# Performance work log

Measured on AMD Instinct MI355X. Metric: run time of the kernel, lower is better.

## Reference

```python
import jax, jax.numpy as jnp
import numpy as np

CHUNK = 64

def _l2norm(x, eps=1e-6):
    return x / jnp.sqrt(jnp.sum(x * x, axis=-1, keepdims=True) + eps)

def setup_inputs() -> dict:
    key = jax.random.key(0)
    ks = jax.random.split(key, 5)
    B, S, H, Dk, Dv = 2, 4096, 16, 128, 128
    q = jax.random.normal(ks[0], (B, S, H, Dk), jnp.float32)
    k = jax.random.normal(ks[1], (B, S, H, Dk), jnp.float32)
    v = jax.random.normal(ks[2], (B, S, H, Dv), jnp.float32)
    g = -jax.random.uniform(ks[3], (B, S, H), jnp.float32)          # log-decay, negative
    beta = jax.random.uniform(ks[4], (B, S, H), jnp.float32)        # (0,1) learning rate
    return {"query": q, "key": k, "value": v, "g": g, "beta": beta}

def reference(query, key, value, g, beta):
    C = CHUNK
    init_dtype = query.dtype
    # [b, s, h, d] -> [b, h, s, d], fp32
    q = jnp.transpose(query, (0, 2, 1, 3)).astype(jnp.float32)
    k = jnp.transpose(key, (0, 2, 1, 3)).astype(jnp.float32)
    v = jnp.transpose(value, (0, 2, 1, 3)).astype(jnp.float32)
    gg = jnp.transpose(g, (0, 2, 1)).astype(jnp.float32)
    bb = jnp.transpose(beta, (0, 2, 1)).astype(jnp.float32)
    # use_qk_l2norm_in_kernel=True
    q = _l2norm(q)
    k = _l2norm(k)
    gg = jnp.clip(gg, -20.0, 20.0)
    B, H, S, Dk = k.shape
    Dv = v.shape[-1]
    pad = (-S) % C
    if pad:
        q = jnp.pad(q, ((0, 0), (0, 0), (0, pad), (0, 0)))
        k = jnp.pad(k, ((0, 0), (0, 0), (0, pad), (0, 0)))
        v = jnp.pad(v, ((0, 0), (0, 0), (0, pad), (0, 0)))
        gg = jnp.pad(gg, ((0, 0), (0, 0), (0, pad)))
        bb = jnp.pad(bb, ((0, 0), (0, 0), (0, pad)))
    T = S + pad
    N = T // C
    q = q * (1.0 / np.sqrt(Dk).astype(np.float32))
    v_beta = v * bb[..., None]
    k_beta = k * bb[..., None]
    # chunk: [b, h, n, c, d]
    qc = q.reshape(B, H, N, C, Dk)
    kc = k.reshape(B, H, N, C, Dk)
    vc = v.reshape(B, H, N, C, Dv)
    kbc = k_beta.reshape(B, H, N, C, Dk)
    vbc = v_beta.reshape(B, H, N, C, Dv)
    gc = jnp.cumsum(gg.reshape(B, H, N, C), axis=-1)
    tril = jnp.tril(jnp.ones((C, C), bool))
    strict = jnp.tril(jnp.ones((C, C), bool), -1)
    # decay_mask[i,j] = exp(g_i - g_j) on lower triangle (incl diag), else 0
    gd = gc[..., :, None] - gc[..., None, :]
    decay = jnp.where(tril, jnp.exp(jnp.where(tril, gd, 0.0)), 0.0)
    # UT transform: torch's in-place row loop computes Tm = (I - A)^{-1} with
    # A = -(k_beta @ k^T * decay) on the strictly lower triangle.
    kk = jnp.einsum('bhnik,bhnjk->bhnij', kbc, kc)
    A = jnp.where(strict, -(kk * decay), 0.0)
    I = jnp.eye(C, dtype=jnp.float32)
    Tm = jax.scipy.linalg.solve_triangular(I - A, jnp.broadcast_to(I, A.shape), lower=True, unit_diagonal=True)
    v_ut = jnp.einsum('bhnij,bhnjd->bhnid', Tm, vbc)
    k_cumdecay = jnp.einsum('bhnij,bhnjd->bhnid', Tm, kbc * jnp.exp(gc)[..., None])
    # sequential inter-chunk recurrence
    xs = tuple(jnp.moveaxis(a, 2, 0) for a in (qc, kc, v_ut, k_cumdecay, gc, decay))
    S0 = jnp.zeros((B, H, Dk, Dv), jnp.float32)
    def step(state, x):
        qi, ki, vi, kci, gi, dmi = x
        attn = jnp.where(tril, jnp.einsum('bhik,bhjk->bhij', qi, ki) * dmi, 0.0)
        v_prime = jnp.einsum('bhik,bhkd->bhid', kci, state)
        v_new = vi - v_prime
        inter = jnp.einsum('bhik,bhkd->bhid', qi * jnp.exp(gi)[..., None], state)
        out = inter + jnp.einsum('bhij,bhjd->bhid', attn, v_new)
        g_last = gi[..., -1]
        k_dec = ki * jnp.exp(g_last[..., None] - gi)[..., None]
        new_state = state * jnp.exp(g_last)[..., None, None] + jnp.einsum('bhik,bhid->bhkd', k_dec, v_new)
        return new_state, out
    _, outs = jax.lax.scan(step, S0, xs)  # outs: [n, b, h, c, dv]
    out = jnp.moveaxis(outs, 0, 2).reshape(B, H, T, Dv)[:, :, :S]
    return jnp.transpose(out, (0, 2, 1, 3)).astype(init_dtype)
```

## Files before the change

### kernel.cpp

```cpp
#include <hip/hip_runtime.h>
#include <math.h>


#define CC 64

constexpr int B_  = 2;
constexpr int S_  = 4096;
constexpr int H_  = 16;
constexpr int DK_ = 128;
constexpr int DV_ = 128;
constexpr int NC_  = S_ / CC;
constexpr int NCH_ = B_ * H_ * NC_;
constexpr int W_   = 16;
constexpr int NWB_ = DV_ / W_;

constexpr float QSCALE = 0.08838834764831845f;

constexpr size_t WS_KCUM = 0;
constexpr size_t WS_VUT  = WS_KCUM + (size_t)NCH_ * CC * DK_;
constexpr size_t WS_ATT  = WS_VUT  + (size_t)NCH_ * CC * DV_;
constexpr size_t WS_GC   = WS_ATT  + (size_t)NCH_ * CC * CC;

__device__ __forceinline__ void ld4(float* d, const float* s) {
    float4 t = *(const float4*)s;
    d[0] = t.x; d[1] = t.y; d[2] = t.z; d[3] = t.w;
}
__device__ __forceinline__ void st4(float* d, const float* s) {
    *(float4*)d = make_float4(s[0], s[1], s[2], s[3]);
}

__global__ __launch_bounds__(512) void gdn_prep(
    const float* __restrict__ q, const float* __restrict__ k,
    const float* __restrict__ v, const float* __restrict__ g,
    const float* __restrict__ beta, float* __restrict__ ws)
{
    const int cid = blockIdx.x;
    const int n   = cid & (NC_ - 1);
    const int bh  = cid / NC_;
    const int h   = bh & (H_ - 1);
    const int b   = bh / H_;
    const int t   = threadIdx.x;
    const int s0  = n * CC;

    __shared__ float s_k[CC][132];
    __shared__ float s_q[CC][132];
    __shared__ float s_A[CC][66];
    __shared__ float s_at[CC][68];
    __shared__ float s_gc[CC];
    __shared__ float s_beta[CC];

    if (t < CC) {
        const size_t gi = ((size_t)b * S_ + s0 + t) * H_ + h;
        float gv = g[gi];
        float x = fminf(fmaxf(gv, -20.f), 20.f);
        s_beta[t] = beta[gi];
#pragma unroll
        for (int o = 1; o < CC; o <<= 1) {
            float y = __shfl_up(x, o);
            if (t >= o) x += y;
        }
        s_gc[t] = x;
    }

    {
        const int i  = t >> 3;
        const int d0 = (t & 7) * 16;
        const size_t rb = (((size_t)b * S_ + s0 + i) * H_ + h) * (size_t)DK_;
        float qr[4][4], kr[4][4];
        float ssq = 0.f, ssk = 0.f;
#pragma unroll
        for (int j4 = 0; j4 < 4; ++j4) {
            ld4(qr[j4], q + rb + d0 + j4 * 4);
            ld4(kr[j4], k + rb + d0 + j4 * 4);
#pragma unroll
            for (int c = 0; c < 4; ++c) { ssq += qr[j4][c] * qr[j4][c]; ssk += kr[j4][c] * kr[j4][c]; }
        }
        ssq += __shfl_xor(ssq, 1); ssq += __shfl_xor(ssq, 2); ssq += __shfl_xor(ssq, 4);
        ssk += __shfl_xor(ssk, 1); ssk += __shfl_xor(ssk, 2); ssk += __shfl_xor(ssk, 4);
        const float rq = QSCALE / sqrtf(ssq + 1e-6f);
        const float rk = 1.0f   / sqrtf(ssk + 1e-6f);
#pragma unroll
        for (int j4 = 0; j4 < 4; ++j4) {
            float tq[4], tk[4];
#pragma unroll
            for (int c = 0; c < 4; ++c) { tq[c] = qr[j4][c] * rq; tk[c] = kr[j4][c] * rk; }
            st4(&s_q[i][d0 + j4 * 4], tq);
            st4(&s_k[i][d0 + j4 * 4], tk);
        }
    }
    __syncthreads();

    {
        const int ks   = t & 1;
        const int slot = t >> 1;
        const int tj = (slot & 7) | (((slot >> 5) & 1) << 3);
        const int ti = ((slot >> 3) & 3) | ((slot >> 6) << 2);
        const int i0 = ti * 4, j0 = tj * 4;
        float dq[4][4] = {}, dkk[4][4] = {};
        if (j0 <= i0 + 3) {
            for (int s = 0; s < 16; ++s) {
                const int dd = (ks + 2 * s) * 4;
                float qa[4][4], ka[4][4], kb[4][4];
#pragma unroll
                for (int r = 0; r < 4; ++r) { ld4(qa[r], &s_q[i0 + r][dd]); ld4(ka[r], &s_k[i0 + r][dd]); }
#pragma unroll
                for (int c = 0; c < 4; ++c) ld4(kb[c], &s_k[j0 + c][dd]);
#pragma unroll
                for (int r = 0; r < 4; ++r)
#pragma unroll
                    for (int c = 0; c < 4; ++c) {
                        dq[r][c]  += qa[r][0]*kb[c][0] + qa[r][1]*kb[c][1] + qa[r][2]*kb[c][2] + qa[r][3]*kb[c][3];
                        dkk[r][c] += ka[r][0]*kb[c][0] + ka[r][1]*kb[c][1] + ka[r][2]*kb[c][2] + ka[r][3]*kb[c][3];
                    }
            }
        }
#pragma unroll
        for (int r = 0; r < 4; ++r)
#pragma unroll
            for (int c = 0; c < 4; ++c) {
                float x = dq[r][c];  x += __shfl_xor(x, 1); dq[r][c] = x;
                float y = dkk[r][c]; y += __shfl_xor(y, 1); dkk[r][c] = y;
            }
#pragma unroll
        for (int r = 0; r < 4; ++r)
#pragma unroll
            for (int cc = 0; cc < 2; ++cc) {
                const int c = ks * 2 + cc;
                const int i = i0 + r, j = j0 + c;
                float av = 0.f;
                if (j <= i) {
                    const float dec = expf(s_gc[i] - s_gc[j]);
                    av = dq[r][c] * dec;
                    if (j < i) s_A[i][j] = -(s_beta[i] * dkk[r][c]) * dec;
                }
                s_at[i][j] = av;
            }
    }
    __syncthreads();

    {
        const size_t vb = (((size_t)b * S_ + s0) * H_ + h) * (size_t)DV_;
#pragma unroll
        for (int r = 0; r < 4; ++r) {
            const int f4i = r * 512 + t;
            const int row = f4i >> 5, c4 = (f4i & 31) * 4;
            float tv[4];
            ld4(tv, v + vb + (size_t)row * H_ * DV_ + c4);
            const float be = s_beta[row];
            tv[0] *= be; tv[1] *= be; tv[2] *= be; tv[3] *= be;
            st4(&s_q[row][c4], tv);
            float tk[4];
            ld4(tk, &s_k[row][c4]);
            const float sc = be * expf(s_gc[row]);
            tk[0] *= sc; tk[1] *= sc; tk[2] *= sc; tk[3] *= sc;
            st4(&s_k[row][c4], tk);
        }
    }
    __syncthreads();

    if (t < 256) {
        const int d = t & 127;
        float* u = (t < 128) ? &s_q[0][0] : &s_k[0][0];
        for (int blk = 0; blk < 16; ++blk) {
            const int i0 = blk * 4;
            const float u0 = u[(i0 + 0) * 132 + d];
            const float u1 = u[(i0 + 1) * 132 + d] + s_A[i0 + 1][i0] * u0;
            const float u2 = u[(i0 + 2) * 132 + d] + s_A[i0 + 2][i0] * u0 + s_A[i0 + 2][i0 + 1] * u1;
            const float u3 = u[(i0 + 3) * 132 + d] + s_A[i0 + 3][i0] * u0 + s_A[i0 + 3][i0 + 1] * u1
                                                   + s_A[i0 + 3][i0 + 2] * u2;
            u[(i0 + 1) * 132 + d] = u1;
            u[(i0 + 2) * 132 + d] = u2;
            u[(i0 + 3) * 132 + d] = u3;
            for (int i = i0 + 4; i < CC; ++i) {
                const float* Ai = s_A[i];
                u[i * 132 + d] += Ai[i0] * u0 + Ai[i0 + 1] * u1 + Ai[i0 + 2] * u2 + Ai[i0 + 3] * u3;
            }
        }
    }
    __syncthreads();

    {
        const size_t kcb = WS_KCUM + (size_t)cid * CC * DK_;
        const size_t vub = WS_VUT  + (size_t)cid * CC * DV_;
#pragma unroll
        for (int r = 0; r < 4; ++r) {
            const int f4i = r * 512 + t;
            const int row = f4i >> 5, c4 = (f4i & 31) * 4;
            float tk[4], tv[4];
            ld4(tk, &s_k[row][c4]);
            ld4(tv, &s_q[row][c4]);
            st4((float*)(ws + kcb) + f4i * 4, tk);
            st4((float*)(ws + vub) + f4i * 4, tv);
        }
        const size_t atb = WS_ATT + (size_t)cid * CC * CC;
#pragma unroll
        for (int r = 0; r < 2; ++r) {
            const int f4i = r * 512 + t;
            const int row = f4i >> 4, c4 = (f4i & 15) * 4;
            float ta[4];
            ld4(ta, &s_at[row][c4]);
            st4((float*)(ws + atb) + f4i * 4, ta);
        }
        if (t < CC) ws[WS_GC + (size_t)cid * CC + t] = s_gc[t];
    }
}

__global__ __launch_bounds__(512) void gdn_scan(
    const float* __restrict__ q, const float* __restrict__ k,
    const float* __restrict__ ws, float* __restrict__ out)
{
    const int bh  = blockIdx.x & 31;
    const int wb  = blockIdx.x >> 5;
    const int h   = bh & (H_ - 1);
    const int b   = bh / H_;
    const int dv0 = wb * W_;
    const int t   = threadIdx.x;

    const int ks   = t & 3;
    const int slot = t >> 2;
    const int jg   = slot & 3;
    const int mg   = slot >> 2;
    const int dp0  = jg * 4;

    __shared__ float s_kq[128][132];
    __shared__ float s_kd[64][132];
    __shared__ float s_at[64][68];
    __shared__ float s_st[128][20];
    __shared__ float s_vn[64][20];
    __shared__ float s_o[64][20];

    for (int p = t; p < 128 * 20; p += 512) (&s_st[0][0])[p] = 0.f;
    __syncthreads();

    for (int n = 0; n < NC_; ++n) {
        const int cid = bh * NC_ + n;
        const int s0  = n * CC;

        const float gl  = ws[WS_GC + (size_t)cid * CC + (CC - 1)];
        const float egl = expf(gl);

        {
            const float* kcb = ws + WS_KCUM + (size_t)cid * CC * DK_;
#pragma unroll
            for (int r = 0; r < 4; ++r) {
                const int f4i = r * 512 + t;
                const int row = f4i >> 5, c4 = (f4i & 31) * 4;
                float tv[4];
                ld4(tv, kcb + f4i * 4);
                st4(&s_kq[row][c4], tv);
            }
            const float* atb = ws + WS_ATT + (size_t)cid * CC * CC;
#pragma unroll
            for (int r = 0; r < 2; ++r) {
                const int f4i = r * 512 + t;
                const int row = f4i >> 4, c4 = (f4i & 15) * 4;
                float tv[4];
                ld4(tv, atb + f4i * 4);
                st4(&s_at[row][c4], tv);
            }
        }

        float vut_[4][4];
        if (ks == 0 && mg < 16) {
            const float* vub = ws + WS_VUT + (size_t)cid * CC * DV_;
            const int i0 = mg * 4;
#pragma unroll
            for (int r = 0; r < 4; ++r) ld4(vut_[r], vub + (size_t)(i0 + r) * DV_ + dv0 + dp0);
        }

        {
            const int i  = t >> 3;
            const int d0 = (t & 7) * 16;
            const float gci = ws[WS_GC + (size_t)cid * CC + i];
            const size_t rb = (((size_t)b * S_ + s0 + i) * H_ + h) * (size_t)DK_;
            float qr[4][4], kr[4][4];
            float ssq = 0.f, ssk = 0.f;
#pragma unroll
            for (int j4 = 0; j4 < 4; ++j4) {
                ld4(qr[j4], q + rb + d0 + j4 * 4);
                ld4(kr[j4], k + rb + d0 + j4 * 4);
#pragma unroll
                for (int c = 0; c < 4; ++c) { ssq += qr[j4][c] * qr[j4][c]; ssk += kr[j4][c] * kr[j4][c]; }
            }
            ssq += __shfl_xor(ssq, 1); ssq += __shfl_xor(ssq, 2); ssq += __shfl_xor(ssq, 4);
            ssk += __shfl_xor(ssk, 1); ssk += __shfl_xor(ssk, 2); ssk += __shfl_xor(ssk, 4);
            const float rq  = QSCALE / sqrtf(ssq + 1e-6f) * expf(gci);
            const float rkd = expf(gl - gci) / sqrtf(ssk + 1e-6f);
#pragma unroll
            for (int j4 = 0; j4 < 4; ++j4) {
                float tq[4], tk[4];
#pragma unroll
                for (int c = 0; c < 4; ++c) { tq[c] = qr[j4][c] * rq; tk[c] = kr[j4][c] * rkd; }
                st4(&s_kq[64 + i][d0 + j4 * 4], tq);
                st4(&s_kd[i][d0 + j4 * 4], tk);
            }
        }
        __syncthreads();

        {
            const int m0 = mg * 4;
            float acc[4][4] = {};
            for (int s = 0; s < 8; ++s) {
                const int dk = (ks + 4 * s) * 4;
                float Bv[4][4], Av[4][4];
#pragma unroll
                for (int kk = 0; kk < 4; ++kk) ld4(Bv[kk], &s_st[dk + kk][dp0]);
#pragma unroll
                for (int r = 0; r < 4; ++r) ld4(Av[r], &s_kq[m0 + r][dk]);
#pragma unroll
                for (int r = 0; r < 4; ++r)
#pragma unroll
                    for (int c = 0; c < 4; ++c)
                        acc[r][c] += Av[r][0]*Bv[0][c] + Av[r][1]*Bv[1][c]
                                   + Av[r][2]*Bv[2][c] + Av[r][3]*Bv[3][c];
            }
#pragma unroll
            for (int r = 0; r < 4; ++r)
#pragma unroll
                for (int c = 0; c < 4; ++c) {
                    float x = acc[r][c];
                    x += __shfl_xor(x, 1); x += __shfl_xor(x, 2);
                    acc[r][c] = x;
                }
            if (ks == 0) {
                if (mg < 16) {
                    const int i0 = mg * 4;
#pragma unroll
                    for (int r = 0; r < 4; ++r) {
                        float tv[4];
#pragma unroll
                        for (int c = 0; c < 4; ++c) tv[c] = vut_[r][c] - acc[r][c];
                        st4(&s_vn[i0 + r][dp0], tv);
                    }
                } else {
                    const int i0 = (mg - 16) * 4;
#pragma unroll
                    for (int r = 0; r < 4; ++r) st4(&s_o[i0 + r][dp0], acc[r]);
                }
            }
        }
        __syncthreads();

        {
            const int i0b = mg * 2;
            float bacc[2][4] = {};
            for (int s = 0; s < 4; ++s) {
                const int j = (ks + 4 * s) * 4;
                float vnv[4][4], atv[2][4];
#pragma unroll
                for (int kk = 0; kk < 4; ++kk) ld4(vnv[kk], &s_vn[j + kk][dp0]);
#pragma unroll
                for (int r = 0; r < 2; ++r) ld4(atv[r], &s_at[i0b + r][j]);
#pragma unroll
                for (int r = 0; r < 2; ++r)
#pragma unroll
                    for (int c = 0; c < 4; ++c)
                        bacc[r][c] += atv[r][0]*vnv[0][c] + atv[r][1]*vnv[1][c]
                                    + atv[r][2]*vnv[2][c] + atv[r][3]*vnv[3][c];
            }
#pragma unroll
            for (int r = 0; r < 2; ++r)
#pragma unroll
                for (int c = 0; c < 4; ++c) {
                    float x = bacc[r][c];
                    x += __shfl_xor(x, 1); x += __shfl_xor(x, 2);
                    bacc[r][c] = x;
                }
            if (ks == 0) {
#pragma unroll
                for (int r = 0; r < 2; ++r) {
                    float ov[4];
                    ld4(ov, &s_o[i0b + r][dp0]);
#pragma unroll
                    for (int c = 0; c < 4; ++c) ov[c] += bacc[r][c];
                    st4(out + (((size_t)b * S_ + s0 + i0b + r) * H_ + h) * (size_t)DV_ + dv0 + dp0, ov);
                }
            }
        }
        {
            const int dk0 = mg * 4;
            float cacc[4][4] = {};
            for (int s = 0; s < 4; ++s) {
                const int ib = (ks + 4 * s) * 4;
#pragma unroll
                for (int kk = 0; kk < 4; ++kk) {
                    float kdv[4], vnv[4];
                    ld4(kdv, &s_kd[ib + kk][dk0]);
                    ld4(vnv, &s_vn[ib + kk][dp0]);
#pragma unroll
                    for (int r = 0; r < 4; ++r)
#pragma unroll
                        for (int c = 0; c < 4; ++c)
                            cacc[r][c] += kdv[r] * vnv[c];
                }
            }
#pragma unroll
            for (int r = 0; r < 4; ++r)
#pragma unroll
                for (int c = 0; c < 4; ++c) {
                    float x = cacc[r][c];
                    x += __shfl_xor(x, 1); x += __shfl_xor(x, 2);
                    cacc[r][c] = x;
                }
            if (ks == 0) {
#pragma unroll
                for (int r = 0; r < 4; ++r) {
                    float st_[4];
                    ld4(st_, &s_st[dk0 + r][dp0]);
#pragma unroll
                    for (int c = 0; c < 4; ++c) st_[c] = st_[c] * egl + cacc[r][c];
                    st4(&s_st[dk0 + r][dp0], st_);
                }
            }
        }
        __syncthreads();
    }
}

extern "C" void kernel_launch(void* const* d_in, const int* in_sizes, int n_in,
                              void* d_out, int out_size, void* d_ws, size_t ws_size,
                              hipStream_t stream) {
    const float* q    = (const float*)d_in[0];
    const float* k    = (const float*)d_in[1];
    const float* v    = (const float*)d_in[2];
    const float* g    = (const float*)d_in[3];
    const float* beta = (const float*)d_in[4];
    float* ws  = (float*)d_ws;
    float* out = (float*)d_out;

    gdn_prep<<<NCH_, 512, 0, stream>>>(q, k, v, g, beta, ws);
    gdn_scan<<<B_ * H_ * NWB_, 512, 0, stream>>>(q, k, ws, out);
}
```

Before: 1.086 ms.

## Software-pipeline next-chunk global loads into registers across the scan loop

The scan loop now issues the global loads for the next chunk (kcumdecay, attention block, raw q/k rows, gc values and v_ut) into registers at the start of the current iteration. It writes them to shared memory only after the barriers that free each buffer, so global memory latency overlaps the current chunk's matmuls instead of stalling the sequential recurrence. The decay factor for the state update is carried across iterations, and the launch bounds now request 2 blocks per CU. The prefetch buffers add a lot of register pressure and may cause spills, especially under the tighter launch bound.

```diff
diff --git a/kernel.cpp b/kernel.cpp
--- a/kernel.cpp
+++ b/kernel.cpp
@@ -205,7 +205,7 @@
     }
 }
 
-__global__ __launch_bounds__(512) void gdn_scan(
+__global__ __launch_bounds__(512, 2) void gdn_scan(
     const float* __restrict__ q, const float* __restrict__ k,
     const float* __restrict__ ws, float* __restrict__ out)
 {
@@ -222,6 +222,9 @@
     const int mg   = slot >> 2;
     const int dp0  = jg * 4;
 
+    const int irow = t >> 3;
+    const int d0   = (t & 7) * 16;
+
     __shared__ float s_kq[128][132];
     __shared__ float s_kd[64][132];
     __shared__ float s_at[64][68];
@@ -229,73 +232,92 @@
     __shared__ float s_vn[64][20];
     __shared__ float s_o[64][20];
 
+    float pf_kc[4][4];
+    float pf_q[4][4], pf_k[4][4];
+    float pf_at[2][4];
+    float vut_[4][4];
+    float gci_n, gl_n;
+    float rkd_sv;
+    float egl_cur;
+
+    auto issue_main = [&](int cc) {
+        const int cid = bh * NC_ + cc;
+        const float* kcb = ws + WS_KCUM + (size_t)cid * CC * DK_;
+#pragma unroll
+        for (int r = 0; r < 4; ++r) ld4(pf_kc[r], kcb + (r * 512 + t) * 4);
+        const float* atb = ws + WS_ATT + (size_t)cid * CC * CC;
+#pragma unroll
+        for (int r = 0; r < 2; ++r) ld4(pf_at[r], atb + (r * 512 + t) * 4);
+        const size_t rb = (((size_t)b * S_ + (size_t)cc * CC + irow) * H_ + h) * (size_t)DK_;
+#pragma unroll
+        for (int j4 = 0; j4 < 4; ++j4) {
+            ld4(pf_q[j4], q + rb + d0 + j4 * 4);
+            ld4(pf_k[j4], k + rb + d0 + j4 * 4);
+        }
+        gci_n = ws[WS_GC + (size_t)cid * CC + irow];
+        gl_n  = ws[WS_GC + (size_t)cid * CC + (CC - 1)];
+    };
+    auto issue_vut = [&](int cc) {
+        if (ks == 0 && mg < 16) {
+            const float* vub = ws + WS_VUT + (size_t)(bh * NC_ + cc) * CC * DV_;
+            const int i0 = mg * 4;
+#pragma unroll
+            for (int r = 0; r < 4; ++r) ld4(vut_[r], vub + (size_t)(i0 + r) * DV_ + dv0 + dp0);
+        }
+    };
+    auto stage_kq = [&]() {
+#pragma unroll
+        for (int r = 0; r < 4; ++r) {
+            const int f4i = r * 512 + t;
+            st4(&s_kq[f4i >> 5][(f4i & 31) * 4], pf_kc[r]);
+        }
+        float ssq = 0.f, ssk = 0.f;
+#pragma unroll
+        for (int j4 = 0; j4 < 4; ++j4)
+#pragma unroll
+            for (int c = 0; c < 4; ++c) {
+                ssq += pf_q[j4][c] * pf_q[j4][c];
+                ssk += pf_k[j4][c] * pf_k[j4][c];
+            }
+        ssq += __shfl_xor(ssq, 1); ssq += __shfl_xor(ssq, 2); ssq += __shfl_xor(ssq, 4);
+        ssk += __shfl_xor(ssk, 1); ssk += __shfl_xor(ssk, 2); ssk += __shfl_xor(ssk, 4);
+        const float rq = QSCALE / sqrtf(ssq + 1e-6f) * expf(gci_n);
+        rkd_sv = expf(gl_n - gci_n) / sqrtf(ssk + 1e-6f);
+#pragma unroll
+        for (int j4 = 0; j4 < 4; ++j4) {
+            float tq[4];
+#pragma unroll
+            for (int c = 0; c < 4; ++c) tq[c] = pf_q[j4][c] * rq;
+            st4(&s_kq[64 + irow][d0 + j4 * 4], tq);
+        }
+    };
+    auto stage_kdat = [&]() {
+#pragma unroll
+        for (int j4 = 0; j4 < 4; ++j4) {
+            float tk[4];
+#pragma unroll
+            for (int c = 0; c < 4; ++c) tk[c] = pf_k[j4][c] * rkd_sv;
+            st4(&s_kd[irow][d0 + j4 * 4], tk);
+        }
+#pragma unroll
+        for (int r = 0; r < 2; ++r) {
+            const int f4i = r * 512 + t;
+            st4(&s_at[f4i >> 4][(f4i & 15) * 4], pf_at[r]);
+        }
+    };
+
     for (int p = t; p < 128 * 20; p += 512) (&s_st[0][0])[p] = 0.f;
+    issue_main(0);
+    issue_vut(0);
+    stage_kq();
+    stage_kdat();
+    egl_cur = expf(gl_n);
     __syncthreads();
 
     for (int n = 0; n < NC_; ++n) {
-        const int cid = bh * NC_ + n;
-        const int s0  = n * CC;
-
-        const float gl  = ws[WS_GC + (size_t)cid * CC + (CC - 1)];
-        const float egl = expf(gl);
-
-        {
-            const float* kcb = ws + WS_KCUM + (size_t)cid * CC * DK_;
-#pragma unroll
-            for (int r = 0; r < 4; ++r) {
-                const int f4i = r * 512 + t;
-                const int row = f4i >> 5, c4 = (f4i & 31) * 4;
-                float tv[4];
-                ld4(tv, kcb + f4i * 4);
-                st4(&s_kq[row][c4], tv);
-            }
-            const float* atb = ws + WS_ATT + (size_t)cid * CC * CC;
-#pragma unroll
-            for (int r = 0; r < 2; ++r) {
-                const int f4i = r * 512 + t;
-                const int row = f4i >> 4, c4 = (f4i & 15) * 4;
-                float tv[4];
-                ld4(tv, atb + f4i * 4);
-                st4(&s_at[row][c4], tv);
-            }
-        }
-
-        float vut_[4][4];
-        if (ks == 0 && mg < 16) {
-            const float* vub = ws + WS_VUT + (size_t)cid * CC * DV_;
-            const int i0 = mg * 4;
-#pragma unroll
-            for (int r = 0; r < 4; ++r) ld4(vut_[r], vub + (size_t)(i0 + r) * DV_ + dv0 + dp0);
-        }
-
-        {
-            const int i  = t >> 3;
-            const int d0 = (t & 7) * 16;
-            const float gci = ws[WS_GC + (size_t)cid * CC + i];
-            const size_t rb = (((size_t)b * S_ + s0 + i) * H_ + h) * (size_t)DK_;
-            float qr[4][4], kr[4][4];
-            float ssq = 0.f, ssk = 0.f;
-#pragma unroll
-            for (int j4 = 0; j4 < 4; ++j4) {
-                ld4(qr[j4], q + rb + d0 + j4 * 4);
-                ld4(kr[j4], k + rb + d0 + j4 * 4);
-#pragma unroll
-                for (int c = 0; c < 4; ++c) { ssq += qr[j4][c] * qr[j4][c]; ssk += kr[j4][c] * kr[j4][c]; }
-            }
-            ssq += __shfl_xor(ssq, 1); ssq += __shfl_xor(ssq, 2); ssq += __shfl_xor(ssq, 4);
-            ssk += __shfl_xor(ssk, 1); ssk += __shfl_xor(ssk, 2); ssk += __shfl_xor(ssk, 4);
-            const float rq  = QSCALE / sqrtf(ssq + 1e-6f) * expf(gci);
-            const float rkd = expf(gl - gci) / sqrtf(ssk + 1e-6f);
-#pragma unroll
-            for (int j4 = 0; j4 < 4; ++j4) {
-                float tq[4], tk[4];
-#pragma unroll
-                for (int c = 0; c < 4; ++c) { tq[c] = qr[j4][c] * rq; tk[c] = kr[j4][c] * rkd; }
-                st4(&s_kq[64 + i][d0 + j4 * 4], tq);
-                st4(&s_kd[i][d0 + j4 * 4], tk);
-            }
-        }
-        __syncthreads();
+        const int s0   = n * CC;
+        const bool more = (n + 1 < NC_);
+        if (more) issue_main(n + 1);
 
         {
             const int m0 = mg * 4;
@@ -339,7 +361,9 @@
                 }
             }
         }
+        if (more) issue_vut(n + 1);
         __syncthreads();
+        if (more) stage_kq();
 
         {
             const int i0b = mg * 2;
@@ -408,12 +432,16 @@
                     float st_[4];
                     ld4(st_, &s_st[dk0 + r][dp0]);
 #pragma unroll
-                    for (int c = 0; c < 4; ++c) st_[c] = st_[c] * egl + cacc[r][c];
+                    for (int c = 0; c < 4; ++c) st_[c] = st_[c] * egl_cur + cacc[r][c];
                     st4(&s_st[dk0 + r][dp0], st_);
                 }
             }
         }
         __syncthreads();
+        if (more) {
+            stage_kdat();
+            egl_cur = expf(gl_n);
+        }
     }
 }
 
```

New measurement: 1.853 ms. 70.6% more time.
